# Optimization experiments

Measured on AMD Instinct MI355X. Metric: run time of the kernel, lower is better.

Reference implementation:

```python
import jax, jax.numpy as jnp
import numpy as np

N_NODES = 50000
N_EDGES = 500000
D_NODE = 128
D_EDGE = 64
D_HID = 256
D_OUT = 64


def setup_inputs() -> dict:
    key = jax.random.key(0)
    k1, k2, k3, k4, k5 = jax.random.split(key, 5)
    node_feats = jax.random.normal(k1, (N_NODES, D_NODE), dtype=jnp.float32)
    edge_index = jax.random.randint(k2, (2, N_EDGES), 0, N_NODES, dtype=jnp.int64)
    edge_attr = jax.random.normal(k3, (N_EDGES, D_EDGE), dtype=jnp.float32)
    d_in = 2 * D_NODE + D_EDGE  # 320
    W1 = jax.random.normal(k4, (d_in, D_HID), dtype=jnp.float32) * (1.0 / np.sqrt(d_in))
    b1 = jnp.zeros((D_HID,), dtype=jnp.float32)
    W2 = jax.random.normal(k5, (D_HID, D_OUT), dtype=jnp.float32) * (1.0 / np.sqrt(D_HID))
    b2 = jnp.zeros((D_OUT,), dtype=jnp.float32)
    return {"node_feats": node_feats, "edge_index": edge_index, "edge_attr": edge_attr,
            "W1": W1, "b1": b1, "W2": W2, "b2": b2}


def reference(node_feats, edge_index, edge_attr, W1, b1, W2, b2):
    row, col = edge_index[0], edge_index[1]
    # irregular gather of endpoint features, concat with edge attrs: [E, 2*d_node + d_edge]
    x = jnp.concatenate([node_feats[row], node_feats[col], edge_attr], axis=1)
    h = jax.nn.relu(x @ W1 + b1)  # [E, D_HID]
    return h @ W2 + b2            # [E, D_OUT]
```

## Files before the change

kernel.cpp:

```cpp
#include <hip/hip_runtime.h>
#include <hip/hip_bf16.h>
#include <stdint.h>

#define E_EDGES 500000
#define NNODES  50000
#define DN 128
#define DE 64
#define DH 256
#define DO 64
#define BE 32
#define TS 528

typedef __attribute__((ext_vector_type(8))) short short8;
typedef __attribute__((ext_vector_type(4))) short short4v;
typedef __attribute__((ext_vector_type(4))) float f32x4;

__device__ __forceinline__ short f2bf(float f) {
    union { __hip_bfloat16 h; short s; } u;
    u.h = __float2bfloat16(f);
    return u.s;
}

__global__ void convert_weights(const float* __restrict__ W1, const float* __restrict__ W2,
                                short* __restrict__ WcatT, short* __restrict__ W1cT,
                                short* __restrict__ W2T) {
    int idx = blockIdx.x * 256 + threadIdx.x;
    if (idx < 512 * 128) {
        int c = idx >> 7, k = idx & 127;
        WcatT[idx] = f2bf(W1[(c < 256 ? k : k + 128) * DH + (c & 255)]);
    } else if (idx < 512 * 128 + 256 * 64) {
        int i = idx - 512 * 128;
        int c = i >> 6, k = i & 63;
        W1cT[i] = f2bf(W1[(256 + k) * DH + c]);
    } else if (idx < 512 * 128 + 256 * 64 + 64 * 256) {
        int i = idx - 512 * 128 - 256 * 64;
        int n = i >> 8, k = i & 255;
        W2T[i] = f2bf(W2[k * DO + n]);
    }
}

__global__ __launch_bounds__(256, 4) void node_gemm(
    const float* __restrict__ nf, const short* __restrict__ WcatT,
    const float* __restrict__ b1, short* __restrict__ PQ)
{
    __shared__ __align__(16) short xt[64 * 128];
    const int tid = threadIdx.x, lane = tid & 63, wv = tid >> 6;
    const int lr = lane & 15, lk = lane >> 4;
    const int r0 = blockIdx.x * 64;
    const int cb = blockIdx.y * 256;
    char* xb = (char*)xt;

    {
        int r = tid >> 2, q = tid & 3;
        int gr = r0 + r; if (gr > NNODES - 1) gr = NNODES - 1;
        const float4* src = (const float4*)(nf + (long)gr * DN) + q * 8;
        #pragma unroll
        for (int i = 0; i < 4; ++i) {
            float4 a = src[2 * i], b = src[2 * i + 1];
            short8 s = { f2bf(a.x), f2bf(a.y), f2bf(a.z), f2bf(a.w),
                         f2bf(b.x), f2bf(b.y), f2bf(b.z), f2bf(b.w) };
            *(short8*)(xb + ((r * 256 + q * 64 + i * 16) ^ ((r & 7) << 4))) = s;
        }
    }
    __syncthreads();

    f32x4 acc[4][4];
    #pragma unroll
    for (int m = 0; m < 4; ++m)
        #pragma unroll
        for (int n = 0; n < 4; ++n)
            acc[m][n] = (f32x4){0.f, 0.f, 0.f, 0.f};

    #pragma unroll
    for (int kt = 0; kt < 4; ++kt) {
        short8 a[4], w[4];
        #pragma unroll
        for (int m = 0; m < 4; ++m) {
            int row = 16 * m + lr;
            a[m] = *(const short8*)(xb + ((row * 256 + kt * 64 + lk * 16) ^ ((row & 7) << 4)));
        }
        #pragma unroll
        for (int n = 0; n < 4; ++n)
            w[n] = *(const short8*)(WcatT + (long)(cb + wv * 64 + n * 16 + lr) * 128 + kt * 32 + lk * 8);
        #pragma unroll
        for (int m = 0; m < 4; ++m)
            #pragma unroll
            for (int n = 0; n < 4; ++n)
                acc[m][n] = __builtin_amdgcn_mfma_f32_16x16x32_bf16(w[n], a[m], acc[m][n], 0, 0, 0);
    }

    #pragma unroll
    for (int m = 0; m < 4; ++m) {
        int row = r0 + 16 * m + lr;
        if (row < NNODES) {
            #pragma unroll
            for (int n = 0; n < 4; ++n) {
                float4 bv = make_float4(0.f, 0.f, 0.f, 0.f);
                if (cb == 0) bv = *(const float4*)(b1 + wv * 64 + n * 16 + lk * 4);
                short4v s = { f2bf(acc[m][n][0] + bv.x), f2bf(acc[m][n][1] + bv.y),
                              f2bf(acc[m][n][2] + bv.z), f2bf(acc[m][n][3] + bv.w) };
                *(short4v*)(PQ + (long)row * 512 + cb + wv * 64 + n * 16 + lk * 4) = s;
            }
        }
    }
}

__global__ __launch_bounds__(256, 4) void edge_mlp(
    const int* __restrict__ eidx, const float* __restrict__ ea,
    const short* __restrict__ PQ, const short* __restrict__ W1cT,
    const short* __restrict__ W2T, const float* __restrict__ b2,
    float* __restrict__ out)
{
    __shared__ __align__(16) char hbuf[32 * TS];

    const int tid = threadIdx.x, lane = tid & 63, wv = tid >> 6;
    const int lr = lane & 15, lk = lane >> 4;
    const long e0 = (long)blockIdx.x * BE;

    const int ri0 = eidx[e0 + lr],      ci0 = eidx[E_EDGES + e0 + lr];
    const int ri1 = eidx[e0 + 16 + lr], ci1 = eidx[E_EDGES + e0 + 16 + lr];

    short8 ifrag;
    #pragma unroll
    for (int i = 0; i < 8; ++i)
        ifrag[i] = (((8 * lk + i) & 15) == lr) ? (short)0x3F80 : (short)0;

    const short* pb0 = (lk < 2) ? (PQ + (long)ri0 * 512 + wv * 64)
                                : (PQ + (long)ci0 * 512 + 256 + wv * 64);
    const short* pb1 = (lk < 2) ? (PQ + (long)ri1 * 512 + wv * 64)
                                : (PQ + (long)ci1 * 512 + 256 + wv * 64);
    short8 pq0[4], pq1[4];
    #pragma unroll
    for (int n = 0; n < 4; ++n) {
        pq0[n] = *(const short8*)(pb0 + n * 16 + (lk & 1) * 8);
        pq1[n] = *(const short8*)(pb1 + n * 16 + (lk & 1) * 8);
    }

    f32x4 acc[2][4];
    #pragma unroll
    for (int m = 0; m < 2; ++m)
        #pragma unroll
        for (int n = 0; n < 4; ++n)
            acc[m][n] = (f32x4){0.f, 0.f, 0.f, 0.f};

    #pragma unroll
    for (int kt = 0; kt < 2; ++kt) {
        short8 w[4], eb[2];
        #pragma unroll
        for (int n = 0; n < 4; ++n)
            w[n] = *(const short8*)(W1cT + (wv * 64 + n * 16 + lr) * 64 + kt * 32 + lk * 8);
        #pragma unroll
        for (int m = 0; m < 2; ++m) {
            const float4* s = (const float4*)(ea + (e0 + 16 * m + lr) * DE + kt * 32 + lk * 8);
            float4 x = s[0], y = s[1];
            eb[m] = (short8){ f2bf(x.x), f2bf(x.y), f2bf(x.z), f2bf(x.w),
                              f2bf(y.x), f2bf(y.y), f2bf(y.z), f2bf(y.w) };
        }
        #pragma unroll
        for (int m = 0; m < 2; ++m)
            #pragma unroll
            for (int n = 0; n < 4; ++n)
                acc[m][n] = __builtin_amdgcn_mfma_f32_16x16x32_bf16(w[n], eb[m], acc[m][n], 0, 0, 0);
    }

    #pragma unroll
    for (int n = 0; n < 4; ++n) {
        acc[0][n] = __builtin_amdgcn_mfma_f32_16x16x32_bf16(ifrag, pq0[n], acc[0][n], 0, 0, 0);
        acc[1][n] = __builtin_amdgcn_mfma_f32_16x16x32_bf16(ifrag, pq1[n], acc[1][n], 0, 0, 0);
    }

    #pragma unroll
    for (int m = 0; m < 2; ++m) {
        const int e = 16 * m + lr;
        #pragma unroll
        for (int n = 0; n < 4; ++n) {
            const int o = 8 * wv + 2 * n + (lk >> 1);
            short4v hs = { f2bf(fmaxf(acc[m][n][0], 0.f)),
                           f2bf(fmaxf(acc[m][n][1], 0.f)),
                           f2bf(fmaxf(acc[m][n][2], 0.f)),
                           f2bf(fmaxf(acc[m][n][3], 0.f)) };
            *(short4v*)(hbuf + o * TS + e * 16 + (lk & 1) * 8) = hs;
        }
    }
    __syncthreads();

    f32x4 acc2[2];
    acc2[0] = (f32x4){0.f, 0.f, 0.f, 0.f};
    acc2[1] = (f32x4){0.f, 0.f, 0.f, 0.f};

    #pragma unroll
    for (int kt = 0; kt < 8; ++kt) {
        short8 w2 = *(const short8*)(W2T + (wv * 16 + lr) * 256 + kt * 32 + lk * 8);
        #pragma unroll
        for (int m = 0; m < 2; ++m) {
            short8 hb = *(const short8*)(hbuf + (4 * kt + lk) * TS + (16 * m + lr) * 16);
            acc2[m] = __builtin_amdgcn_mfma_f32_16x16x32_bf16(w2, hb, acc2[m], 0, 0, 0);
        }
    }

    float4 bb = *(const float4*)(b2 + wv * 16 + lk * 4);
    #pragma unroll
    for (int m = 0; m < 2; ++m) {
        long ge = e0 + 16 * m + lr;
        float4 o;
        o.x = acc2[m][0] + bb.x;
        o.y = acc2[m][1] + bb.y;
        o.z = acc2[m][2] + bb.z;
        o.w = acc2[m][3] + bb.w;
        *(float4*)(out + ge * DO + wv * 16 + lk * 4) = o;
    }
}

extern "C" void kernel_launch(void* const* d_in, const int* in_sizes, int n_in,
                              void* d_out, int out_size, void* d_ws, size_t ws_size,
                              hipStream_t stream) {
    const float* node_feats = (const float*)d_in[0];
    const int*   eidx       = (const int*)d_in[1];
    const float* edge_attr  = (const float*)d_in[2];
    const float* W1         = (const float*)d_in[3];
    const float* b1         = (const float*)d_in[4];
    const float* W2         = (const float*)d_in[5];
    const float* b2         = (const float*)d_in[6];
    float* out = (float*)d_out;

    short* WcatT = (short*)d_ws;
    short* W1cT  = WcatT + 512 * 128;
    short* W2T   = W1cT + 256 * 64;
    short* PQ    = W2T + 64 * 256;

    convert_weights<<<384, 256, 0, stream>>>(W1, W2, WcatT, W1cT, W2T);
    node_gemm<<<dim3(782, 2), 256, 0, stream>>>(node_feats, WcatT, b1, PQ);
    edge_mlp<<<E_EDGES / BE, 256, 0, stream>>>(eidx, edge_attr, PQ, W1cT, W2T, b2, out);
}
```

Measured before the change: 310.1 us.

## Process two edge tiles per block with prefetched gathers and double hbuf

Each edge_mlp block now handles two 32-edge tiles. The second tile's gathers are issued before the first tile's hidden activations are written, and both tiles share one barrier and one W2 pass through a doubled LDS buffer. The aim is to hide gather latency, amortise the W2/W1c weight loads and bias load, and halve the block count. In exchange the kernel uses more registers and twice the LDS per block, which may lower occupancy under launch_bounds(256,4).

```diff
diff --git a/kernel.cpp b/kernel.cpp
--- a/kernel.cpp
+++ b/kernel.cpp
@@ -9,6 +9,8 @@
 #define DH 256
 #define DO 64
 #define BE 32
+#define NTILES (E_EDGES / BE)
+#define NBLK ((NTILES + 1) / 2)
 #define TS 528
 
 typedef __attribute__((ext_vector_type(8))) short short8;
@@ -111,104 +113,144 @@
     const short* __restrict__ W2T, const float* __restrict__ b2,
     float* __restrict__ out)
 {
-    __shared__ __align__(16) char hbuf[32 * TS];
+    __shared__ __align__(16) char hbuf[2][32 * TS];
 
     const int tid = threadIdx.x, lane = tid & 63, wv = tid >> 6;
     const int lr = lane & 15, lk = lane >> 4;
-    const long e0 = (long)blockIdx.x * BE;
-
-    const int ri0 = eidx[e0 + lr],      ci0 = eidx[E_EDGES + e0 + lr];
-    const int ri1 = eidx[e0 + 16 + lr], ci1 = eidx[E_EDGES + e0 + 16 + lr];
 
     short8 ifrag;
     #pragma unroll
     for (int i = 0; i < 8; ++i)
         ifrag[i] = (((8 * lk + i) & 15) == lr) ? (short)0x3F80 : (short)0;
 
-    const short* pb0 = (lk < 2) ? (PQ + (long)ri0 * 512 + wv * 64)
-                                : (PQ + (long)ci0 * 512 + 256 + wv * 64);
-    const short* pb1 = (lk < 2) ? (PQ + (long)ri1 * 512 + wv * 64)
-                                : (PQ + (long)ci1 * 512 + 256 + wv * 64);
-    short8 pq0[4], pq1[4];
-    #pragma unroll
-    for (int n = 0; n < 4; ++n) {
-        pq0[n] = *(const short8*)(pb0 + n * 16 + (lk & 1) * 8);
-        pq1[n] = *(const short8*)(pb1 + n * 16 + (lk & 1) * 8);
+    const float4 bb = *(const float4*)(b2 + wv * 16 + lk * 4);
+
+    const long t0 = 2L * blockIdx.x;
+    const bool has1 = (t0 + 1 < NTILES);
+    const long e0 = t0 * BE;
+    const long e1 = e0 + (has1 ? BE : 0);
+
+#define LOAD_TILE(E, PQF, EBF)                                                    \
+    {                                                                             \
+        const int ri0 = eidx[(E) + lr],      ci0 = eidx[E_EDGES + (E) + lr];      \
+        const int ri1 = eidx[(E) + 16 + lr], ci1 = eidx[E_EDGES + (E) + 16 + lr]; \
+        const short* pb0 = (lk < 2) ? (PQ + (long)ri0 * 512 + wv * 64)            \
+                                    : (PQ + (long)ci0 * 512 + 256 + wv * 64);     \
+        const short* pb1 = (lk < 2) ? (PQ + (long)ri1 * 512 + wv * 64)            \
+                                    : (PQ + (long)ci1 * 512 + 256 + wv * 64);     \
+        _Pragma("unroll")                                                         \
+        for (int n = 0; n < 4; ++n) {                                             \
+            PQF[0][n] = *(const short8*)(pb0 + n * 16 + (lk & 1) * 8);            \
+            PQF[1][n] = *(const short8*)(pb1 + n * 16 + (lk & 1) * 8);            \
+        }                                                                         \
+        _Pragma("unroll")                                                         \
+        for (int m = 0; m < 2; ++m)                                               \
+            _Pragma("unroll")                                                     \
+            for (int kt = 0; kt < 2; ++kt) {                                      \
+                const float4* s = (const float4*)(ea + ((E) + 16 * m + lr) * DE + kt * 32 + lk * 8); \
+                float4 x = s[0], y = s[1];                                        \
+                EBF[m][kt] = (short8){ f2bf(x.x), f2bf(x.y), f2bf(x.z), f2bf(x.w),\
+                                       f2bf(y.x), f2bf(y.y), f2bf(y.z), f2bf(y.w) }; \
+            }                                                                     \
+    }
+
+#define COMP_TILE(PQF, EBF, ACC)                                                  \
+    {                                                                             \
+        const f32x4 zz = (f32x4){0.f, 0.f, 0.f, 0.f};                             \
+        _Pragma("unroll")                                                         \
+        for (int n = 0; n < 4; ++n) {                                             \
+            ACC[0][n] = __builtin_amdgcn_mfma_f32_16x16x32_bf16(ifrag, PQF[0][n], zz, 0, 0, 0); \
+            ACC[1][n] = __builtin_amdgcn_mfma_f32_16x16x32_bf16(ifrag, PQF[1][n], zz, 0, 0, 0); \
+        }                                                                         \
+        _Pragma("unroll")                                                         \
+        for (int kt = 0; kt < 2; ++kt) {                                          \
+            short8 w[4];                                                          \
+            _Pragma("unroll")                                                     \
+            for (int n = 0; n < 4; ++n)                                           \
+                w[n] = *(const short8*)(W1cT + (wv * 64 + n * 16 + lr) * 64 + kt * 32 + lk * 8); \
+            _Pragma("unroll")                                                     \
+            for (int m = 0; m < 2; ++m)                                           \
+                _Pragma("unroll")                                                 \
+                for (int n = 0; n < 4; ++n)                                       \
+                    ACC[m][n] = __builtin_amdgcn_mfma_f32_16x16x32_bf16(w[n], EBF[m][kt], ACC[m][n], 0, 0, 0); \
+        }                                                                         \
+    }
+
+#define HWRITE(ACC, BUF)                                                          \
+    _Pragma("unroll")                                                             \
+    for (int m = 0; m < 2; ++m) {                                                 \
+        const int e = 16 * m + lr;                                                \
+        _Pragma("unroll")                                                         \
+        for (int n = 0; n < 4; ++n) {                                             \
+            const int o = 8 * wv + 2 * n + (lk >> 1);                             \
+            short4v hs = { f2bf(fmaxf(ACC[m][n][0], 0.f)),                        \
+                           f2bf(fmaxf(ACC[m][n][1], 0.f)),                        \
+                           f2bf(fmaxf(ACC[m][n][2], 0.f)),                        \
+                           f2bf(fmaxf(ACC[m][n][3], 0.f)) };                      \
+            *(short4v*)((BUF) + o * TS + e * 16 + (lk & 1) * 8) = hs;             \
+        }                                                                         \
     }
 
     f32x4 acc[2][4];
-    #pragma unroll
-    for (int m = 0; m < 2; ++m)
-        #pragma unroll
-        for (int n = 0; n < 4; ++n)
-            acc[m][n] = (f32x4){0.f, 0.f, 0.f, 0.f};
-
-    #pragma unroll
-    for (int kt = 0; kt < 2; ++kt) {
-        short8 w[4], eb[2];
-        #pragma unroll
-        for (int n = 0; n < 4; ++n)
-            w[n] = *(const short8*)(W1cT + (wv * 64 + n * 16 + lr) * 64 + kt * 32 + lk * 8);
-        #pragma unroll
-        for (int m = 0; m < 2; ++m) {
-            const float4* s = (const float4*)(ea + (e0 + 16 * m + lr) * DE + kt * 32 + lk * 8);
-            float4 x = s[0], y = s[1];
-            eb[m] = (short8){ f2bf(x.x), f2bf(x.y), f2bf(x.z), f2bf(x.w),
-                              f2bf(y.x), f2bf(y.y), f2bf(y.z), f2bf(y.w) };
-        }
+    {
+        short8 pqf[2][4], ebf[2][2];
+        LOAD_TILE(e0, pqf, ebf)
+        COMP_TILE(pqf, ebf, acc)
+    }
+    {
+        short8 pqg[2][4], ebg[2][2];
+        LOAD_TILE(e1, pqg, ebg)
+        HWRITE(acc, hbuf[0])
+        COMP_TILE(pqg, ebg, acc)
+        HWRITE(acc, hbuf[1])
+    }
+
+    __syncthreads();
+
+    f32x4 acc2[2][2];
+    #pragma unroll
+    for (int t = 0; t < 2; ++t)
         #pragma unroll
         for (int m = 0; m < 2; ++m)
-            #pragma unroll
-            for (int n = 0; n < 4; ++n)
-                acc[m][n] = __builtin_amdgcn_mfma_f32_16x16x32_bf16(w[n], eb[m], acc[m][n], 0, 0, 0);
-    }
-
-    #pragma unroll
-    for (int n = 0; n < 4; ++n) {
-        acc[0][n] = __builtin_amdgcn_mfma_f32_16x16x32_bf16(ifrag, pq0[n], acc[0][n], 0, 0, 0);
-        acc[1][n] = __builtin_amdgcn_mfma_f32_16x16x32_bf16(ifrag, pq1[n], acc[1][n], 0, 0, 0);
-    }
-
-    #pragma unroll
-    for (int m = 0; m < 2; ++m) {
-        const int e = 16 * m + lr;
-        #pragma unroll
-        for (int n = 0; n < 4; ++n) {
-            const int o = 8 * wv + 2 * n + (lk >> 1);
-            short4v hs = { f2bf(fmaxf(acc[m][n][0], 0.f)),
-                           f2bf(fmaxf(acc[m][n][1], 0.f)),
-                           f2bf(fmaxf(acc[m][n][2], 0.f)),
-                           f2bf(fmaxf(acc[m][n][3], 0.f)) };
-            *(short4v*)(hbuf + o * TS + e * 16 + (lk & 1) * 8) = hs;
-        }
-    }
-    __syncthreads();
-
-    f32x4 acc2[2];
-    acc2[0] = (f32x4){0.f, 0.f, 0.f, 0.f};
-    acc2[1] = (f32x4){0.f, 0.f, 0.f, 0.f};
+            acc2[t][m] = (f32x4){0.f, 0.f, 0.f, 0.f};
 
     #pragma unroll
     for (int kt = 0; kt < 8; ++kt) {
         short8 w2 = *(const short8*)(W2T + (wv * 16 + lr) * 256 + kt * 32 + lk * 8);
         #pragma unroll
         for (int m = 0; m < 2; ++m) {
-            short8 hb = *(const short8*)(hbuf + (4 * kt + lk) * TS + (16 * m + lr) * 16);
-            acc2[m] = __builtin_amdgcn_mfma_f32_16x16x32_bf16(w2, hb, acc2[m], 0, 0, 0);
-        }
-    }
-
-    float4 bb = *(const float4*)(b2 + wv * 16 + lk * 4);
+            short8 h0 = *(const short8*)(hbuf[0] + (4 * kt + lk) * TS + (16 * m + lr) * 16);
+            acc2[0][m] = __builtin_amdgcn_mfma_f32_16x16x32_bf16(w2, h0, acc2[0][m], 0, 0, 0);
+            short8 h1 = *(const short8*)(hbuf[1] + (4 * kt + lk) * TS + (16 * m + lr) * 16);
+            acc2[1][m] = __builtin_amdgcn_mfma_f32_16x16x32_bf16(w2, h1, acc2[1][m], 0, 0, 0);
+        }
+    }
+
     #pragma unroll
     for (int m = 0; m < 2; ++m) {
         long ge = e0 + 16 * m + lr;
         float4 o;
-        o.x = acc2[m][0] + bb.x;
-        o.y = acc2[m][1] + bb.y;
-        o.z = acc2[m][2] + bb.z;
-        o.w = acc2[m][3] + bb.w;
+        o.x = acc2[0][m][0] + bb.x;
+        o.y = acc2[0][m][1] + bb.y;
+        o.z = acc2[0][m][2] + bb.z;
+        o.w = acc2[0][m][3] + bb.w;
         *(float4*)(out + ge * DO + wv * 16 + lk * 4) = o;
     }
+    if (has1) {
+        #pragma unroll
+        for (int m = 0; m < 2; ++m) {
+            long ge = e1 + 16 * m + lr;
+            float4 o;
+            o.x = acc2[1][m][0] + bb.x;
+            o.y = acc2[1][m][1] + bb.y;
+            o.z = acc2[1][m][2] + bb.z;
+            o.w = acc2[1][m][3] + bb.w;
+            *(float4*)(out + ge * DO + wv * 16 + lk * 4) = o;
+        }
+    }
+#undef LOAD_TILE
+#undef COMP_TILE
+#undef HWRITE
 }
 
 extern "C" void kernel_launch(void* const* d_in, const int* in_sizes, int n_in,
@@ -230,5 +272,5 @@
 
     convert_weights<<<384, 256, 0, stream>>>(W1, W2, WcatT, W1cT, W2T);
     node_gemm<<<dim3(782, 2), 256, 0, stream>>>(node_feats, WcatT, b1, PQ);
-    edge_mlp<<<E_EDGES / BE, 256, 0, stream>>>(eidx, edge_attr, PQ, W1cT, W2T, b2, out);
-}
+    edge_mlp<<<NBLK, 256, 0, stream>>>(eidx, edge_attr, PQ, W1cT, W2T, b2, out);
+}
```

New measurement: 272.1 us. 1.14x faster.

## Fuse edge MLP per wave with shuffle-based hidden transfer, removing shared memory

Applied to the files above, without the earlier changes.

The edge kernel is reorganized so each wavefront independently handles 16 edges across all 256 hidden units. The first layer is computed in 16-column chunks and fed straight into the second-layer MFMAs, with cross-lane shuffles reshaping the hidden activations instead of a shared-memory round trip and block barrier. This removes LDS traffic and __syncthreads and lets waves run independently. In exchange, each wave now reads all of W1c and W2 (more cache/global weight traffic per edge), issues many more shuffles, and does less reuse of weight fragments across edges.

```diff
diff --git a/kernel.cpp b/kernel.cpp
--- a/kernel.cpp
+++ b/kernel.cpp
@@ -8,8 +8,7 @@
 #define DE 64
 #define DH 256
 #define DO 64
-#define BE 32
-#define TS 528
+#define NWAVES (E_EDGES / 16)
 
 typedef __attribute__((ext_vector_type(8))) short short8;
 typedef __attribute__((ext_vector_type(4))) short short4v;
@@ -19,6 +18,9 @@
     union { __hip_bfloat16 h; short s; } u;
     u.h = __float2bfloat16(f);
     return u.s;
+}
+__device__ __forceinline__ uint32_t pack2bf(float a, float b) {
+    return (uint32_t)(uint16_t)f2bf(a) | ((uint32_t)(uint16_t)f2bf(b) << 16);
 }
 
 __global__ void convert_weights(const float* __restrict__ W1, const float* __restrict__ W2,
@@ -105,109 +107,94 @@
     }
 }
 
-__global__ __launch_bounds__(256, 4) void edge_mlp(
+__global__ __launch_bounds__(256, 4) void edge_fused(
     const int* __restrict__ eidx, const float* __restrict__ ea,
     const short* __restrict__ PQ, const short* __restrict__ W1cT,
     const short* __restrict__ W2T, const float* __restrict__ b2,
     float* __restrict__ out)
 {
-    __shared__ __align__(16) char hbuf[32 * TS];
-
-    const int tid = threadIdx.x, lane = tid & 63, wv = tid >> 6;
+    const int tid = threadIdx.x, lane = tid & 63;
+    const int w = blockIdx.x * 4 + (tid >> 6);
+    if (w >= NWAVES) return;
     const int lr = lane & 15, lk = lane >> 4;
-    const long e0 = (long)blockIdx.x * BE;
-
-    const int ri0 = eidx[e0 + lr],      ci0 = eidx[E_EDGES + e0 + lr];
-    const int ri1 = eidx[e0 + 16 + lr], ci1 = eidx[E_EDGES + e0 + 16 + lr];
+    const long e0 = (long)w * 16;
 
     short8 ifrag;
     #pragma unroll
     for (int i = 0; i < 8; ++i)
         ifrag[i] = (((8 * lk + i) & 15) == lr) ? (short)0x3F80 : (short)0;
 
-    const short* pb0 = (lk < 2) ? (PQ + (long)ri0 * 512 + wv * 64)
-                                : (PQ + (long)ci0 * 512 + 256 + wv * 64);
-    const short* pb1 = (lk < 2) ? (PQ + (long)ri1 * 512 + wv * 64)
-                                : (PQ + (long)ci1 * 512 + 256 + wv * 64);
-    short8 pq0[4], pq1[4];
-    #pragma unroll
-    for (int n = 0; n < 4; ++n) {
-        pq0[n] = *(const short8*)(pb0 + n * 16 + (lk & 1) * 8);
-        pq1[n] = *(const short8*)(pb1 + n * 16 + (lk & 1) * 8);
-    }
-
-    f32x4 acc[2][4];
-    #pragma unroll
-    for (int m = 0; m < 2; ++m)
-        #pragma unroll
-        for (int n = 0; n < 4; ++n)
-            acc[m][n] = (f32x4){0.f, 0.f, 0.f, 0.f};
-
-    #pragma unroll
-    for (int kt = 0; kt < 2; ++kt) {
-        short8 w[4], eb[2];
-        #pragma unroll
-        for (int n = 0; n < 4; ++n)
-            w[n] = *(const short8*)(W1cT + (wv * 64 + n * 16 + lr) * 64 + kt * 32 + lk * 8);
-        #pragma unroll
-        for (int m = 0; m < 2; ++m) {
-            const float4* s = (const float4*)(ea + (e0 + 16 * m + lr) * DE + kt * 32 + lk * 8);
-            float4 x = s[0], y = s[1];
-            eb[m] = (short8){ f2bf(x.x), f2bf(x.y), f2bf(x.z), f2bf(x.w),
-                              f2bf(y.x), f2bf(y.y), f2bf(y.z), f2bf(y.w) };
-        }
-        #pragma unroll
-        for (int m = 0; m < 2; ++m)
+    const int ri = eidx[e0 + lr];
+    const int ci = eidx[E_EDGES + e0 + lr];
+
+    const short* pqb = (lk < 2) ? (PQ + (long)ri * 512 + 8 * (lk & 1))
+                                : (PQ + (long)ci * 512 + 256 + 8 * (lk & 1));
+
+    short8 eaf[2];
+    {
+        const float* eap = ea + (e0 + lr) * DE + 8 * lk;
+        #pragma unroll
+        for (int kt = 0; kt < 2; ++kt) {
+            float4 x = *(const float4*)(eap + 32 * kt);
+            float4 y = *(const float4*)(eap + 32 * kt + 4);
+            eaf[kt] = (short8){ f2bf(x.x), f2bf(x.y), f2bf(x.z), f2bf(x.w),
+                                f2bf(y.x), f2bf(y.y), f2bf(y.z), f2bf(y.w) };
+        }
+    }
+
+    f32x4 acc2[4];
+    #pragma unroll
+    for (int n2 = 0; n2 < 4; ++n2) acc2[n2] = (f32x4){0.f, 0.f, 0.f, 0.f};
+
+    const f32x4 zz = (f32x4){0.f, 0.f, 0.f, 0.f};
+    const int sA = lr + 32 * (lk & 1);
+    const int sB = sA + 16;
+    const bool hi = (lk >= 2);
+
+    #pragma unroll
+    for (int nt = 0; nt < 8; ++nt) {
+        uint2 h[2];
+        #pragma unroll
+        for (int p = 0; p < 2; ++p) {
+            const int n = 2 * nt + p;
+            short8 pq = *(const short8*)(pqb + 16 * n);
+            f32x4 a = __builtin_amdgcn_mfma_f32_16x16x32_bf16(ifrag, pq, zz, 0, 0, 0);
             #pragma unroll
-            for (int n = 0; n < 4; ++n)
-                acc[m][n] = __builtin_amdgcn_mfma_f32_16x16x32_bf16(w[n], eb[m], acc[m][n], 0, 0, 0);
-    }
-
-    #pragma unroll
-    for (int n = 0; n < 4; ++n) {
-        acc[0][n] = __builtin_amdgcn_mfma_f32_16x16x32_bf16(ifrag, pq0[n], acc[0][n], 0, 0, 0);
-        acc[1][n] = __builtin_amdgcn_mfma_f32_16x16x32_bf16(ifrag, pq1[n], acc[1][n], 0, 0, 0);
-    }
-
-    #pragma unroll
-    for (int m = 0; m < 2; ++m) {
-        const int e = 16 * m + lr;
-        #pragma unroll
-        for (int n = 0; n < 4; ++n) {
-            const int o = 8 * wv + 2 * n + (lk >> 1);
-            short4v hs = { f2bf(fmaxf(acc[m][n][0], 0.f)),
-                           f2bf(fmaxf(acc[m][n][1], 0.f)),
-                           f2bf(fmaxf(acc[m][n][2], 0.f)),
-                           f2bf(fmaxf(acc[m][n][3], 0.f)) };
-            *(short4v*)(hbuf + o * TS + e * 16 + (lk & 1) * 8) = hs;
-        }
-    }
-    __syncthreads();
-
-    f32x4 acc2[2];
-    acc2[0] = (f32x4){0.f, 0.f, 0.f, 0.f};
-    acc2[1] = (f32x4){0.f, 0.f, 0.f, 0.f};
-
-    #pragma unroll
-    for (int kt = 0; kt < 8; ++kt) {
-        short8 w2 = *(const short8*)(W2T + (wv * 16 + lr) * 256 + kt * 32 + lk * 8);
-        #pragma unroll
-        for (int m = 0; m < 2; ++m) {
-            short8 hb = *(const short8*)(hbuf + (4 * kt + lk) * TS + (16 * m + lr) * 16);
-            acc2[m] = __builtin_amdgcn_mfma_f32_16x16x32_bf16(w2, hb, acc2[m], 0, 0, 0);
-        }
-    }
-
-    float4 bb = *(const float4*)(b2 + wv * 16 + lk * 4);
-    #pragma unroll
-    for (int m = 0; m < 2; ++m) {
-        long ge = e0 + 16 * m + lr;
+            for (int kt = 0; kt < 2; ++kt) {
+                short8 w1 = *(const short8*)(W1cT + (16 * n + lr) * 64 + 32 * kt + 8 * lk);
+                a = __builtin_amdgcn_mfma_f32_16x16x32_bf16(w1, eaf[kt], a, 0, 0, 0);
+            }
+            h[p].x = pack2bf(fmaxf(a[0], 0.f), fmaxf(a[1], 0.f));
+            h[p].y = pack2bf(fmaxf(a[2], 0.f), fmaxf(a[3], 0.f));
+        }
+
+        int x0A = __shfl((int)h[0].x, sA), y0A = __shfl((int)h[0].y, sA);
+        int x1A = __shfl((int)h[1].x, sA), y1A = __shfl((int)h[1].y, sA);
+        int x0B = __shfl((int)h[0].x, sB), y0B = __shfl((int)h[0].y, sB);
+        int x1B = __shfl((int)h[1].x, sB), y1B = __shfl((int)h[1].y, sB);
+        union { int i[4]; short8 s; } hb;
+        hb.i[0] = hi ? x1A : x0A;
+        hb.i[1] = hi ? y1A : y0A;
+        hb.i[2] = hi ? x1B : x0B;
+        hb.i[3] = hi ? y1B : y0B;
+
+        #pragma unroll
+        for (int n2 = 0; n2 < 4; ++n2) {
+            short8 w2 = *(const short8*)(W2T + (16 * n2 + lr) * 256 + 32 * nt + 8 * lk);
+            acc2[n2] = __builtin_amdgcn_mfma_f32_16x16x32_bf16(w2, hb.s, acc2[n2], 0, 0, 0);
+        }
+    }
+
+    float* op = out + (e0 + lr) * DO;
+    #pragma unroll
+    for (int n2 = 0; n2 < 4; ++n2) {
+        float4 bb = *(const float4*)(b2 + 16 * n2 + 4 * lk);
         float4 o;
-        o.x = acc2[m][0] + bb.x;
-        o.y = acc2[m][1] + bb.y;
-        o.z = acc2[m][2] + bb.z;
-        o.w = acc2[m][3] + bb.w;
-        *(float4*)(out + ge * DO + wv * 16 + lk * 4) = o;
+        o.x = acc2[n2][0] + bb.x;
+        o.y = acc2[n2][1] + bb.y;
+        o.z = acc2[n2][2] + bb.z;
+        o.w = acc2[n2][3] + bb.w;
+        *(float4*)(op + 16 * n2 + 4 * lk) = o;
     }
 }
 
@@ -230,5 +217,5 @@
 
     convert_weights<<<384, 256, 0, stream>>>(W1, W2, WcatT, W1cT, W2T);
     node_gemm<<<dim3(782, 2), 256, 0, stream>>>(node_feats, WcatT, b1, PQ);
-    edge_mlp<<<E_EDGES / BE, 256, 0, stream>>>(eidx, edge_attr, PQ, W1cT, W2T, b2, out);
-}
+    edge_fused<<<(NWAVES + 3) / 4, 256, 0, stream>>>(eidx, edge_attr, PQ, W1cT, W2T, b2, out);
+}
```

After: 352.6 us. 1.14x slower.
